# Kernel optimization log

Hardware: AMD Instinct MI355X
Metric: run time of the kernel (lower is better)

The kernel has to match this reference:

```python
import jax, jax.numpy as jnp
import numpy as np

VOCAB = 512
EMB = 256
HID = 64
T_HORIZON = 0.05


def setup_inputs() -> dict:
    key = jax.random.key(0)
    ks = jax.random.split(key, 6)
    B, L = 32, 4096
    x = jax.random.randint(ks[0], (B, L), 0, VOCAB, dtype=jnp.int64 if jax.config.jax_enable_x64 else jnp.int32)
    emb_table = jax.random.normal(ks[1], (VOCAB, EMB), dtype=jnp.float32)
    W1 = jax.random.normal(ks[2], (EMB, HID), dtype=jnp.float32) * (1.0 / np.sqrt(EMB))
    b1 = jnp.zeros((HID,), dtype=jnp.float32)
    W2 = jax.random.normal(ks[3], (HID, VOCAB), dtype=jnp.float32) * (1.0 / np.sqrt(HID))
    b2 = jnp.full((VOCAB,), 0.1, dtype=jnp.float32)  # torch: bias.data.fill_(0.1)
    return {"x": x, "emb_table": emb_table, "W1": W1, "b1": b1, "W2": W2, "b2": b2, "steps": 5}


def reference(x, emb_table, W1, b1, W2, b2, steps):
    """Vectorized Gillespie-style Markov jump simulation.

    Equivalent to the torch loop: intensity is computed once per step from the
    current state, then every (b, l) position samples a candidate next state
    from softmax(intensity) with the self-transition zeroed and renormalized
    (== categorical over logits with the current state masked to -inf), and
    accepts it with prob 1 - exp(-rate * dt).
    """
    V = emb_table.shape[0]
    dt = T_HORIZON / steps
    key = jax.random.key(42)
    keys = jax.random.split(key, steps)
    vocab_ids = jnp.arange(V)

    def step(x_t, k):
        # intensity: [B, L, V]
        h = jax.nn.relu(emb_table[x_t] @ W1 + b1)
        intensity = h @ W2 + b2
        # mask self-transition (softmax * (1 - onehot) then renormalize)
        self_mask = x_t[..., None] == vocab_ids  # [B, L, V] bool
        masked_logits = jnp.where(self_mask, -jnp.inf, intensity)
        k1, k2 = jax.random.split(k)
        next_state = jax.random.categorical(k1, masked_logits)  # [B, L]
        rate = jnp.take_along_axis(intensity, next_state[..., None], axis=-1)[..., 0]
        accept_prob = 1.0 - jnp.exp(-rate * dt)
        u = jax.random.uniform(k2, x_t.shape, dtype=rate.dtype)
        x_t = jnp.where(u < accept_prob, next_state.astype(x_t.dtype), x_t)
        return x_t, None

    x_final, _ = jax.lax.scan(step, x, keys)
    return x_final
```

## Files before the change

kernel.cpp:

```cpp
#include <hip/hip_runtime.h>
#include <stdint.h>


#define VOCAB  512
#define EMB    256
#define HID    64
#define NPOS   (32 * 4096)
#define STEPS  5
#define PPW    8
#define CHUNKS (NPOS / PPW)

__host__ __device__ __forceinline__ void tf2x32(uint32_t k0, uint32_t k1,
                                                uint32_t x0, uint32_t x1,
                                                uint32_t& o0, uint32_t& o1) {
  uint32_t ks2 = k0 ^ k1 ^ 0x1BD11BDAu;
  x0 += k0; x1 += k1;
#define TFR(r) { x0 += x1; x1 = (x1 << (r)) | (x1 >> (32 - (r))); x1 ^= x0; }
  TFR(13) TFR(15) TFR(26) TFR(6)
  x0 += k1;  x1 += ks2 + 1u;
  TFR(17) TFR(29) TFR(16) TFR(24)
  x0 += ks2; x1 += k0 + 2u;
  TFR(13) TFR(15) TFR(26) TFR(6)
  x0 += k0;  x1 += k1 + 3u;
  TFR(17) TFR(29) TFR(16) TFR(24)
  x0 += k1;  x1 += ks2 + 4u;
  TFR(13) TFR(15) TFR(26) TFR(6)
  x0 += ks2; x1 += k0 + 5u;
#undef TFR
  o0 = x0; o1 = x1;
}

struct Keys {
  uint32_t k1a[STEPS], k1b[STEPS];
  uint32_t k2a[STEPS], k2b[STEPS];
};

__global__ __launch_bounds__(512)
void build_table(const float* __restrict__ emb,
                 const float* __restrict__ W1,
                 const float* __restrict__ b1,
                 const float* __restrict__ W2,
                 const float* __restrict__ b2,
                 float* __restrict__ I,
                 float* __restrict__ pthr) {
  const int s   = blockIdx.x;
  const int tid = threadIdx.x;
  __shared__ double part[8][HID];
  __shared__ double hd[HID];
  __shared__ float  redmax[8];

  const int hid = tid & (HID - 1);
  const int kq  = tid >> 6;
  const float* e = emb + s * EMB;
  double acc = 0.0;
#pragma unroll
  for (int k = kq; k < EMB; k += 8)
    acc += (double)e[k] * (double)W1[k * HID + hid];
  part[kq][hid] = acc;
  __syncthreads();
  if (kq == 0) {
    const double a = ((part[0][hid] + part[1][hid]) + (part[2][hid] + part[3][hid]))
                   + ((part[4][hid] + part[5][hid]) + (part[6][hid] + part[7][hid]));
    const float m = (float)a + b1[hid];
    hd[hid] = (double)(m > 0.0f ? m : 0.0f);
  }
  __syncthreads();

  double acc2 = 0.0;
#pragma unroll
  for (int k = 0; k < HID; ++k)
    acc2 += hd[k] * (double)W2[k * VOCAB + tid];
  const float val = (float)acc2 + b2[tid];
  I[s * VOCAB + tid] = val;

  float lmax = val;
  for (int off = 32; off > 0; off >>= 1)
    lmax = fmaxf(lmax, __shfl_xor(lmax, off, 64));
  if ((tid & 63) == 0) redmax[tid >> 6] = lmax;
  __syncthreads();
  if (tid == 0) {
    float m = redmax[0];
#pragma unroll
    for (int i = 1; i < 8; ++i) m = fmaxf(m, redmax[i]);
    const float z = (-m) * 0.01f;
    pthr[s] = 1.0f - (float)exp((double)z);
  }
}

__global__ __launch_bounds__(128, 4)
void markov_kernel(const int* __restrict__ x_in,
                   const float* __restrict__ I,
                   const float* __restrict__ pthr,
                   int* __restrict__ x_out,
                   Keys K) {
  const int lane  = threadIdx.x & 63;
  const int chunk = (blockIdx.x << 1) | (threadIdx.x >> 6);
  const int base  = chunk * PPW;
  const int qp = lane / 5;
  const int qt = lane - qp * 5;
  const float TINYF = 1.17549435e-38f;

  int scur = (lane < PPW) ? x_in[base + lane] : 0;

  float u40 = 0.0f;
  if (lane < PPW * STEPS) {
    uint32_t w0, w1;
    tf2x32(K.k2a[qt], K.k2b[qt], 0u, (uint32_t)(base + qp), w0, w1);
    u40 = __uint_as_float((((w0 ^ w1) >> 9) | 0x3f800000u)) - 1.0f;
  }

  const int s_of_q = __shfl(scur, qp, 64);
  const bool cand = (lane < PPW * STEPS) && (u40 < pthr[s_of_q]);
  unsigned long long mask = __ballot(cand);

  while (mask) {
    const int q = (int)__builtin_ctzll(mask);
    mask &= mask - 1;
    const int p = q / 5;
    const int t = q - p * 5;
    const int s = __builtin_amdgcn_readfirstlane(__shfl(scur, p, 64));

    const float* row = I + s * VOCAB;
    float rv[8];
#pragma unroll
    for (int j = 0; j < 8; ++j)
      rv[j] = row[lane + (j << 6)];

    const uint32_t fbase = ((uint32_t)(base + p) << 9) + (uint32_t)lane;
    uint32_t bits[8];
#pragma unroll
    for (int j = 0; j < 8; ++j) {
      uint32_t w0, w1;
      tf2x32(K.k1a[t], K.k1b[t], 0u, fbase + ((uint32_t)j << 6), w0, w1);
      bits[j] = w0 ^ w1;
    }

    float best = -__builtin_inff();
    int bidx = 0;
#pragma unroll
    for (int j = 0; j < 8; ++j) {
      float ufv = __uint_as_float((bits[j] >> 9) | 0x3f800000u) - 1.0f;
      if (ufv == 0.0f) ufv = TINYF;
      const float g = -logf(-logf(ufv));
      const int v = lane + (j << 6);
      if (v != s) {
        const float val = rv[j] + g;
        if (val > best) { best = val; bidx = v; }
      }
    }
    for (int off = 32; off > 0; off >>= 1) {
      const float ob = __shfl_xor(best, off, 64);
      const int   oi = __shfl_xor(bidx, off, 64);
      if (ob > best || (ob == best && oi < bidx)) { best = ob; bidx = oi; }
    }
    bidx = __builtin_amdgcn_readfirstlane(bidx);
    const float rate = row[bidx];
    const float z = (-rate) * 0.01f;
    const float pacc = 1.0f - (float)exp((double)z);
    const float u = __shfl(u40, q, 64);
    if (u < pacc) {
      if (lane == p) scur = bidx;
      const unsigned long long fut =
          (((1ull << (p * 5 + 5)) - 1) & ~((1ull << (q + 1)) - 1));
      const float pnew = pthr[bidx];
      const unsigned long long nb = __ballot(u40 < pnew) & fut;
      mask = (mask & ~fut) | nb;
    }
  }
  if (lane < PPW) x_out[base + lane] = scur;
}

extern "C" void kernel_launch(void* const* d_in, const int* in_sizes, int n_in,
                              void* d_out, int out_size, void* d_ws, size_t ws_size,
                              hipStream_t stream) {
  const int*   x   = (const int*)d_in[0];
  const float* emb = (const float*)d_in[1];
  const float* W1  = (const float*)d_in[2];
  const float* b1  = (const float*)d_in[3];
  const float* W2  = (const float*)d_in[4];
  const float* b2  = (const float*)d_in[5];
  float* I    = (float*)d_ws;
  float* pthr = (float*)d_ws + VOCAB * VOCAB;
  int* out = (int*)d_out;

  Keys K;
  for (int t = 0; t < STEPS; ++t) {
    uint32_t Sa, Sb;
    tf2x32(0u, 42u, 0u, (uint32_t)t, Sa, Sb);
    tf2x32(Sa, Sb, 0u, 0u, K.k1a[t], K.k1b[t]);
    tf2x32(Sa, Sb, 0u, 1u, K.k2a[t], K.k2b[t]);
  }

  build_table<<<VOCAB, 512, 0, stream>>>(emb, W1, b1, W2, b2, I, pthr);
  markov_kernel<<<CHUNKS / 2, 128, 0, stream>>>(x, I, pthr, out, K);
}
```

Measured before the change: 116.0 us.

## Batch loads in table build and process two chunks per wave in markov kernel

The table-build kernel now loads 16 weight values into registers before the double-precision FMAs, so more loads can be in flight. The Markov kernel switches to 256-thread blocks with 8192 waves, each looping over two chunks. The pthr lookup is moved to one load per position instead of one per lane. The accepted rate now comes with the argmax reduction, which removes a dependent global load. This adds register pressure and halves the wave count, which could reduce latency hiding.

```diff
diff --git a/kernel.cpp b/kernel.cpp
--- a/kernel.cpp
+++ b/kernel.cpp
@@ -9,6 +9,7 @@
 #define STEPS  5
 #define PPW    8
 #define CHUNKS (NPOS / PPW)
+#define NWAVE  8192
 
 __host__ __device__ __forceinline__ void tf2x32(uint32_t k0, uint32_t k1,
                                                 uint32_t x0, uint32_t x1,
@@ -54,8 +55,18 @@
   const float* e = emb + s * EMB;
   double acc = 0.0;
 #pragma unroll
-  for (int k = kq; k < EMB; k += 8)
-    acc += (double)e[k] * (double)W1[k * HID + hid];
+  for (int ib = 0; ib < 32; ib += 16) {
+    float ev[16], wv[16];
+#pragma unroll
+    for (int i = 0; i < 16; ++i) {
+      const int k = kq + 8 * (ib + i);
+      ev[i] = e[k];
+      wv[i] = W1[k * HID + hid];
+    }
+#pragma unroll
+    for (int i = 0; i < 16; ++i)
+      acc += (double)ev[i] * (double)wv[i];
+  }
   part[kq][hid] = acc;
   __syncthreads();
   if (kq == 0) {
@@ -68,8 +79,15 @@
 
   double acc2 = 0.0;
 #pragma unroll
-  for (int k = 0; k < HID; ++k)
-    acc2 += hd[k] * (double)W2[k * VOCAB + tid];
+  for (int kb = 0; kb < HID; kb += 16) {
+    float wv[16];
+#pragma unroll
+    for (int i = 0; i < 16; ++i)
+      wv[i] = W2[(kb + i) * VOCAB + tid];
+#pragma unroll
+    for (int i = 0; i < 16; ++i)
+      acc2 += hd[kb + i] * (double)wv[i];
+  }
   const float val = (float)acc2 + b2[tid];
   I[s * VOCAB + tid] = val;
 
@@ -87,87 +105,96 @@
   }
 }
 
-__global__ __launch_bounds__(128, 4)
+__global__ __launch_bounds__(256)
 void markov_kernel(const int* __restrict__ x_in,
                    const float* __restrict__ I,
                    const float* __restrict__ pthr,
                    int* __restrict__ x_out,
                    Keys K) {
-  const int lane  = threadIdx.x & 63;
-  const int chunk = (blockIdx.x << 1) | (threadIdx.x >> 6);
-  const int base  = chunk * PPW;
+  const int lane = threadIdx.x & 63;
+  const int wid  = (blockIdx.x << 2) | (threadIdx.x >> 6);
   const int qp = lane / 5;
   const int qt = lane - qp * 5;
   const float TINYF = 1.17549435e-38f;
 
-  int scur = (lane < PPW) ? x_in[base + lane] : 0;
-
-  float u40 = 0.0f;
-  if (lane < PPW * STEPS) {
-    uint32_t w0, w1;
-    tf2x32(K.k2a[qt], K.k2b[qt], 0u, (uint32_t)(base + qp), w0, w1);
-    u40 = __uint_as_float((((w0 ^ w1) >> 9) | 0x3f800000u)) - 1.0f;
-  }
-
-  const int s_of_q = __shfl(scur, qp, 64);
-  const bool cand = (lane < PPW * STEPS) && (u40 < pthr[s_of_q]);
-  unsigned long long mask = __ballot(cand);
-
-  while (mask) {
-    const int q = (int)__builtin_ctzll(mask);
-    mask &= mask - 1;
-    const int p = q / 5;
-    const int t = q - p * 5;
-    const int s = __builtin_amdgcn_readfirstlane(__shfl(scur, p, 64));
-
-    const float* row = I + s * VOCAB;
-    float rv[8];
-#pragma unroll
-    for (int j = 0; j < 8; ++j)
-      rv[j] = row[lane + (j << 6)];
-
-    const uint32_t fbase = ((uint32_t)(base + p) << 9) + (uint32_t)lane;
-    uint32_t bits[8];
-#pragma unroll
-    for (int j = 0; j < 8; ++j) {
+#pragma unroll
+  for (int c = 0; c < 2; ++c) {
+    const int base = (wid + (c << 13)) * PPW;
+
+    int scur = (lane < PPW) ? x_in[base + lane] : 0;
+    const float pv = (lane < PPW) ? pthr[scur] : 0.0f;
+
+    float u40 = 0.0f;
+    if (lane < PPW * STEPS) {
       uint32_t w0, w1;
-      tf2x32(K.k1a[t], K.k1b[t], 0u, fbase + ((uint32_t)j << 6), w0, w1);
-      bits[j] = w0 ^ w1;
+      tf2x32(K.k2a[qt], K.k2b[qt], 0u, (uint32_t)(base + qp), w0, w1);
+      u40 = __uint_as_float((((w0 ^ w1) >> 9) | 0x3f800000u)) - 1.0f;
     }
 
-    float best = -__builtin_inff();
-    int bidx = 0;
-#pragma unroll
-    for (int j = 0; j < 8; ++j) {
-      float ufv = __uint_as_float((bits[j] >> 9) | 0x3f800000u) - 1.0f;
-      if (ufv == 0.0f) ufv = TINYF;
-      const float g = -logf(-logf(ufv));
-      const int v = lane + (j << 6);
-      if (v != s) {
-        const float val = rv[j] + g;
-        if (val > best) { best = val; bidx = v; }
+    const float pq = __shfl(pv, qp, 64);
+    const bool cand = (lane < PPW * STEPS) && (u40 < pq);
+    unsigned long long mask = __ballot(cand);
+
+    while (mask) {
+      const int q = (int)__builtin_ctzll(mask);
+      mask &= mask - 1;
+      const int p = q / 5;
+      const int t = q - p * 5;
+      const int s = __builtin_amdgcn_readfirstlane(__shfl(scur, p, 64));
+
+      const float* row = I + s * VOCAB;
+      float rv[8];
+#pragma unroll
+      for (int j = 0; j < 8; ++j)
+        rv[j] = row[lane + (j << 6)];
+
+      const uint32_t fbase = ((uint32_t)(base + p) << 9) + (uint32_t)lane;
+      uint32_t bits[8];
+#pragma unroll
+      for (int j = 0; j < 8; ++j) {
+        uint32_t w0, w1;
+        tf2x32(K.k1a[t], K.k1b[t], 0u, fbase + ((uint32_t)j << 6), w0, w1);
+        bits[j] = w0 ^ w1;
+      }
+
+      float best = -__builtin_inff();
+      float rbest = 0.0f;
+      int bidx = 0;
+#pragma unroll
+      for (int j = 0; j < 8; ++j) {
+        float ufv = __uint_as_float((bits[j] >> 9) | 0x3f800000u) - 1.0f;
+        if (ufv == 0.0f) ufv = TINYF;
+        const float g = -logf(-logf(ufv));
+        const int v = lane + (j << 6);
+        if (v != s) {
+          const float val = rv[j] + g;
+          if (val > best) { best = val; bidx = v; rbest = rv[j]; }
+        }
+      }
+      for (int off = 32; off > 0; off >>= 1) {
+        const float ob = __shfl_xor(best, off, 64);
+        const int   oi = __shfl_xor(bidx, off, 64);
+        const float orv = __shfl_xor(rbest, off, 64);
+        if (ob > best || (ob == best && oi < bidx)) {
+          best = ob; bidx = oi; rbest = orv;
+        }
+      }
+      bidx = __builtin_amdgcn_readfirstlane(bidx);
+      const float rate = rbest;
+      const float z = (-rate) * 0.01f;
+      const float pacc = 1.0f - (float)exp((double)z);
+      const float u = __shfl(u40, q, 64);
+      if (u < pacc) {
+        if (lane == p) scur = bidx;
+        const unsigned long long fut =
+            (((1ull << (p * 5 + 5)) - 1) & ~((1ull << (q + 1)) - 1));
+        const float pnew = pthr[bidx];
+        const unsigned long long nb = __ballot(u40 < pnew) & fut;
+        mask = (mask & ~fut) | nb;
       }
     }
-    for (int off = 32; off > 0; off >>= 1) {
-      const float ob = __shfl_xor(best, off, 64);
-      const int   oi = __shfl_xor(bidx, off, 64);
-      if (ob > best || (ob == best && oi < bidx)) { best = ob; bidx = oi; }
-    }
-    bidx = __builtin_amdgcn_readfirstlane(bidx);
-    const float rate = row[bidx];
-    const float z = (-rate) * 0.01f;
-    const float pacc = 1.0f - (float)exp((double)z);
-    const float u = __shfl(u40, q, 64);
-    if (u < pacc) {
-      if (lane == p) scur = bidx;
-      const unsigned long long fut =
-          (((1ull << (p * 5 + 5)) - 1) & ~((1ull << (q + 1)) - 1));
-      const float pnew = pthr[bidx];
-      const unsigned long long nb = __ballot(u40 < pnew) & fut;
-      mask = (mask & ~fut) | nb;
-    }
-  }
-  if (lane < PPW) x_out[base + lane] = scur;
+    if (lane < PPW) x_out[base + lane] = scur;
+  }
 }
 
 extern "C" void kernel_launch(void* const* d_in, const int* in_sizes, int n_in,
@@ -192,5 +219,5 @@
   }
 
   build_table<<<VOCAB, 512, 0, stream>>>(emb, W1, b1, W2, b2, I, pthr);
-  markov_kernel<<<CHUNKS / 2, 128, 0, stream>>>(x, I, pthr, out, K);
-}
+  markov_kernel<<<NWAVE / 4, 256, 0, stream>>>(x, I, pthr, out, K);
+}
```

Measured after the change: 117.6 us. Within noise of the previous version (+1.4%).
